# Kernel optimization log

Measured on AMD Instinct MI355X. Metric: run time of the kernel, lower is better.

The kernel has to match this reference:

```python
import jax, jax.numpy as jnp
import numpy as np
from functools import partial

REGION_NUM = 5
ALPHA = 0.02


def _otsu(u8, N):
    """Per-batch Otsu threshold. u8: (B, N) int32 in [0,255] -> (B,) int32.
    Matches cv2.THRESH_OTSU: argmax over t of between-class variance with
    class0 = bins <= t, binarization is pixel > t."""
    B = u8.shape[0]
    hist = jnp.zeros((B, 256), jnp.float32).at[jnp.arange(B)[:, None], u8].add(1.0)
    p = hist / N
    bins = jnp.arange(256, dtype=jnp.float32)
    w0 = jnp.cumsum(p, axis=1)                 # class-0 mass up to bin t
    mu = jnp.cumsum(p * bins, axis=1)          # class-0 first moment
    mu_t = mu[:, -1:]                          # total mean
    sigma_b = (mu_t * w0 - mu) ** 2 / (w0 * (1.0 - w0) + 1e-12)
    return jnp.argmax(sigma_b, axis=1)         # first max, like OpenCV


def _cc_label(mask):
    """8-connected components via iterative min-label propagation.
    mask: (H, W) bool -> (H, W) int32 labels; 0 = background, components get
    the (min flat index + 1) of their pixels as a unique id in 1..N."""
    H, W = mask.shape
    N = H * W
    BIG = jnp.int32(N + 1)
    idx = jnp.arange(1, N + 1, dtype=jnp.int32).reshape(H, W)
    lab0 = jnp.where(mask, idx, BIG)

    def step(l):
        p = jnp.pad(l, 1, constant_values=N + 1)
        nb = jnp.stack([p[i:i + H, j:j + W] for i in range(3) for j in range(3)])
        return jnp.where(mask, jnp.min(nb, axis=0), BIG)

    def cond(s):
        _, changed, it = s
        return changed & (it < N)

    def body(s):
        l, _, it = s
        nl = step(l)
        return (nl, jnp.any(nl != l), it + 1)

    lab, _, _ = jax.lax.while_loop(cond, body, (lab0, jnp.bool_(True), jnp.int32(0)))
    return jnp.where(mask, lab, 0)


def _forward(z, query_z):
    B, N, D = z.shape
    H = W = int(round(N ** 0.5))
    K = REGION_NUM - 1

    # similarity score + per-batch min-max normalization
    sim = jnp.einsum('bd,bnd->bn', query_z[:, 0], z) / (D ** 0.5)   # (B, N)
    smin = jnp.min(sim, axis=1, keepdims=True)
    smax = jnp.max(sim, axis=1, keepdims=True)
    sal = (sim - smin) / (smax - smin + 1e-6)
    sal = jax.lax.stop_gradient(sal)  # torch detaches before the numpy/cv2 pipeline

    # uint8 quantization (truncation, like .astype(np.uint8)) + Otsu binarization
    u8 = jnp.clip(jnp.floor(sal * 255.0), 0, 255).astype(jnp.int32)
    t = _otsu(u8, N)                              # (B,)
    binary = u8 > t[:, None]                      # (B, N) bool

    # connected components per image
    labels = jax.vmap(_cc_label)(binary.reshape(B, H, W)).reshape(B, N)  # 0..N

    # per-component area and mean saliency
    seg = partial(jax.ops.segment_sum, num_segments=N + 1)
    area = jax.vmap(seg)(jnp.ones((B, N), jnp.float32), labels)   # (B, N+1)
    ssum = jax.vmap(seg)(sal, labels)                              # (B, N+1)
    mean = ssum / jnp.maximum(area, 1.0)

    # keep components with area >= ALPHA*N (label 0 = non-mask excluded)
    valid = (area >= ALPHA * N) & (jnp.arange(N + 1) > 0)
    cand = jnp.where(valid, mean, -jnp.inf)

    # top-(region_num-1) components by mean saliency
    top_s, top_l = jax.lax.top_k(cand, K)         # (B, K)
    sel = jnp.isfinite(top_s)                     # (B, K)
    region = (labels[:, None, :] == top_l[:, :, None]) & sel[:, :, None]  # (B, K, N)
    bg = ~jnp.any(region, axis=1)                 # background = complement of union
    return jnp.concatenate([region, bg[:, None, :]], axis=1).astype(z.dtype)


def setup_inputs() -> dict:
    key = jax.random.key(0)
    k1, k2 = jax.random.split(key)
    B, N, D = 64, 1024, 768
    return {
        'z': jax.random.normal(k1, (B, N, D), dtype=jnp.float32),
        'query_z': jax.random.normal(k2, (B, 1, D), dtype=jnp.float32),
    }


def reference(z, query_z):
    return _forward(z, query_z)
```

## Files before the change

### kernel.cpp

```cpp
#include <hip/hip_runtime.h>
#include <stdint.h>

#define NB   64
#define NPIX 1024
#define DIM  768
#define KTOP 4

__global__ __launch_bounds__(256) void sgatt_sim(const float* __restrict__ z,
                                                 const float* __restrict__ q,
                                                 float* __restrict__ sim) {
    const int b    = blockIdx.y;
    const int lane = threadIdx.x & 63;
    const int wave = threadIdx.x >> 6;
    const float4* qv = reinterpret_cast<const float4*>(q + (size_t)b * DIM);
    const float4 q0 = qv[lane], q1 = qv[lane + 64], q2 = qv[lane + 128];
    const float rt = sqrtf((float)DIM);
#pragma unroll
    for (int r = 0; r < 4; ++r) {
        const int row = blockIdx.x * 16 + wave * 4 + r;
        const float4* zv =
            reinterpret_cast<const float4*>(z + (size_t)(b * NPIX + row) * DIM);
        const float4 z0 = zv[lane], z1 = zv[lane + 64], z2 = zv[lane + 128];
        double acc = (double)z0.x * q0.x + (double)z0.y * q0.y +
                     (double)z0.z * q0.z + (double)z0.w * q0.w;
        acc += (double)z1.x * q1.x + (double)z1.y * q1.y +
               (double)z1.z * q1.z + (double)z1.w * q1.w;
        acc += (double)z2.x * q2.x + (double)z2.y * q2.y +
               (double)z2.z * q2.z + (double)z2.w * q2.w;
#pragma unroll
        for (int o = 32; o > 0; o >>= 1) acc += __shfl_xor(acc, o);
        if (lane == 0) sim[b * NPIX + row] = (float)acc / rt;
    }
}

__device__ inline int uf_find(volatile int* p, int x) {
    int px = p[x];
    while (px != x) {
        const int g = p[px];
        if (g != px) p[x] = g;
        x = g;
        px = p[x];
    }
    return x;
}

__device__ inline void uf_union(volatile int* p, int a, int b) {
    while (true) {
        a = uf_find(p, a);
        b = uf_find(p, b);
        if (a == b) return;
        const int hi = a > b ? a : b;
        const int lo = a ^ b ^ hi;
        const int old = atomicCAS((int*)&p[hi], hi, lo);
        if (old == hi) return;
        a = old; b = lo;
    }
}

__global__ __launch_bounds__(256) void sgatt_region(const float* __restrict__ sim,
                                                    float* __restrict__ out) {
    const int b    = blockIdx.x;
    const int t    = threadIdx.x;
    const int lane = t & 63;
    const int wid  = t >> 6;

    __shared__ int   s_bufA[NPIX];
    __shared__ int   s_bufB[NPIX];
    __shared__ float s_wA[4], s_wB[4];
    __shared__ float s_avv[4];
    __shared__ int   s_avi[4];
    __shared__ float s_smin, s_smax;
    __shared__ int   s_thr;
    __shared__ int   s_top[KTOP];

    s_bufB[t] = 0;
    if (t < NPIX / 32) s_bufB[256 + t] = 0;
    int* s_hist = s_bufB;
    unsigned int* s_mbits = reinterpret_cast<unsigned int*>(s_bufB + 256);

    const float4 sv4 =
        reinterpret_cast<const float4*>(sim + (size_t)b * NPIX)[t];
    const float svj[4] = {sv4.x, sv4.y, sv4.z, sv4.w};
    float mn = fminf(fminf(svj[0], svj[1]), fminf(svj[2], svj[3]));
    float mx = fmaxf(fmaxf(svj[0], svj[1]), fmaxf(svj[2], svj[3]));
#pragma unroll
    for (int o = 32; o > 0; o >>= 1) {
        mn = fminf(mn, __shfl_xor(mn, o));
        mx = fmaxf(mx, __shfl_xor(mx, o));
    }
    if (lane == 0) { s_wA[wid] = mn; s_wB[wid] = mx; }
    __syncthreads();
    if (t == 0) {
        float a = s_wA[0], c = s_wB[0];
        for (int w = 1; w < 4; ++w) { a = fminf(a, s_wA[w]); c = fmaxf(c, s_wB[w]); }
        s_smin = a; s_smax = c;
    }
    __syncthreads();

    const float smin = s_smin;
    const float den0 = __fadd_rn(__fsub_rn(s_smax, smin), 1e-6f);
    float salj[4];
    int u8j[4];
#pragma unroll
    for (int j = 0; j < 4; ++j) {
        salj[j] = __fdiv_rn(__fsub_rn(svj[j], smin), den0);
        int u = (int)floorf(__fmul_rn(salj[j], 255.0f));
        u8j[j] = min(max(u, 0), 255);
        atomicAdd(&s_hist[u8j[j]], 1);
    }
    __syncthreads();

    {
        const float p = __fmul_rn((float)s_hist[t], 1.0f / 1024.0f);
        float w0 = p;
        float mu = __fmul_rn(p, (float)t);
#pragma unroll
        for (int o = 1; o < 64; o <<= 1) {
            const float aw = __shfl_up(w0, o);
            const float am = __shfl_up(mu, o);
            if (lane >= o) { w0 = __fadd_rn(w0, aw); mu = __fadd_rn(mu, am); }
        }
        if (lane == 63) { s_wA[wid] = w0; s_wB[wid] = mu; }
        __syncthreads();
        float mut = 0.0f;
        for (int w = 0; w < 4; ++w) mut = __fadd_rn(mut, s_wB[w]);
        for (int w = 0; w < wid; ++w) {
            w0 = __fadd_rn(w0, s_wA[w]);
            mu = __fadd_rn(mu, s_wB[w]);
        }
        const float num = __fsub_rn(__fmul_rn(mut, w0), mu);
        const float dn  = __fadd_rn(__fmul_rn(w0, __fsub_rn(1.0f, w0)), 1e-12f);
        float v  = __fdiv_rn(__fmul_rn(num, num), dn);
        int   idx = t;
#pragma unroll
        for (int o = 32; o > 0; o >>= 1) {
            const float v2 = __shfl_xor(v, o);
            const int   i2 = __shfl_xor(idx, o);
            if (v2 > v || (v2 == v && i2 < idx)) { v = v2; idx = i2; }
        }
        if (lane == 0) { s_avv[wid] = v; s_avi[wid] = idx; }
    }
    __syncthreads();
    if (t == 0) {
        float bv = s_avv[0]; int bi = s_avi[0];
        for (int w = 1; w < 4; ++w)
            if (s_avv[w] > bv || (s_avv[w] == bv && s_avi[w] < bi)) {
                bv = s_avv[w]; bi = s_avi[w];
            }
        s_thr = bi;
    }
    __syncthreads();
    const int thr = s_thr;

    int* s_par = s_bufA;
    int mj[4];
#pragma unroll
    for (int j = 0; j < 4; ++j) {
        const int px = 4*t + j;
        mj[j] = (u8j[j] > thr) ? 1 : 0;
        s_par[px] = (j > 0 && mj[j] && mj[j-1]) ? (px - 1) : px;
        if (mj[j]) atomicOr(&s_mbits[px >> 5], 1u << (px & 31));
    }
    __syncthreads();

#pragma unroll
    for (int j = 0; j < 4; ++j) {
        if (!mj[j]) continue;
        const int px = 4*t + j;
        const int r = px >> 5, c = px & 31;
#define ONMASK(p) ((s_mbits[(p) >> 5] >> ((p) & 31)) & 1u)
        if (j == 0 && c > 0 && ONMASK(px - 1)) uf_union(s_par, px, px - 1);
        if (r > 0) {
            if (c > 0 && ONMASK(px - 33)) uf_union(s_par, px, px - 33);
            if (ONMASK(px - 32))          uf_union(s_par, px, px - 32);
            if (c < 31 && ONMASK(px - 31)) uf_union(s_par, px, px - 31);
        }
#undef ONMASK
    }
    __syncthreads();

    int labj[4];
    {
        int cur[4], par[4];
#pragma unroll
        for (int j = 0; j < 4; ++j) cur[j] = 4*t + j;
#pragma unroll
        for (int j = 0; j < 4; ++j) par[j] = s_par[cur[j]];
        while (true) {
            bool any = false;
#pragma unroll
            for (int j = 0; j < 4; ++j) any |= (par[j] != cur[j]);
            if (!any) break;
#pragma unroll
            for (int j = 0; j < 4; ++j) cur[j] = par[j];
#pragma unroll
            for (int j = 0; j < 4; ++j) par[j] = s_par[cur[j]];
        }
#pragma unroll
        for (int j = 0; j < 4; ++j) labj[j] = mj[j] ? (cur[j] + 1) : 0;
    }
    __syncthreads();

    float* s_ssum = reinterpret_cast<float*>(s_bufA);
    int*   s_area = s_bufB;
#pragma unroll
    for (int j = 0; j < 4; ++j) { s_area[4*t + j] = 0; s_ssum[4*t + j] = 0.0f; }
    __syncthreads();
#pragma unroll
    for (int j = 0; j < 4; ++j) {
        if (mj[j]) {
            atomicAdd(&s_area[labj[j] - 1], 1);
            atomicAdd(&s_ssum[labj[j] - 1], salj[j]);
        }
    }
    __syncthreads();

    if (wid == 0) {
        unsigned long long key[16];
#pragma unroll
        for (int i = 0; i < 16; ++i) {
            const int idx = lane * 16 + i;
            const int a = s_area[idx];
            key[i] = 0ull;
            if (a >= 21) {
                const float mean = __fdiv_rn(s_ssum[idx], (float)a);
                key[i] = ((unsigned long long)__float_as_uint(mean) << 32) |
                         (unsigned long long)(0xFFFFFFFFu - (unsigned)(idx + 1));
            }
        }
        for (int k = 0; k < KTOP; ++k) {
            unsigned long long v = key[0];
#pragma unroll
            for (int i = 1; i < 16; ++i) v = (key[i] > v) ? key[i] : v;
#pragma unroll
            for (int o = 32; o > 0; o >>= 1) {
                const unsigned long long w = __shfl_xor(v, o);
                if (w > v) v = w;
            }
            if (lane == 0)
                s_top[k] = (v != 0ull)
                               ? (int)(0xFFFFFFFFu - (unsigned)(v & 0xFFFFFFFFull))
                               : -1;
#pragma unroll
            for (int i = 0; i < 16; ++i)
                if (key[i] == v && v != 0ull) key[i] = 0ull;
        }
    }
    __syncthreads();

    float* ob = out + (size_t)b * 5 * NPIX;
    int anyr[4] = {0, 0, 0, 0};
#pragma unroll
    for (int k = 0; k < KTOP; ++k) {
        const int tl = s_top[k];
        float4 o;
        float* op = reinterpret_cast<float*>(&o);
#pragma unroll
        for (int j = 0; j < 4; ++j) {
            const int match = (tl >= 0 && labj[j] == tl) ? 1 : 0;
            anyr[j] |= match;
            op[j] = (float)match;
        }
        reinterpret_cast<float4*>(ob + (size_t)k * NPIX)[t] = o;
    }
    {
        float4 o;
        float* op = reinterpret_cast<float*>(&o);
#pragma unroll
        for (int j = 0; j < 4; ++j) op[j] = anyr[j] ? 0.0f : 1.0f;
        reinterpret_cast<float4*>(ob + (size_t)KTOP * NPIX)[t] = o;
    }
}

extern "C" void kernel_launch(void* const* d_in, const int* in_sizes, int n_in,
                              void* d_out, int out_size, void* d_ws, size_t ws_size,
                              hipStream_t stream) {
    const float* z = (const float*)d_in[0];
    const float* q = (const float*)d_in[1];
    float* out = (float*)d_out;
    float* sim = (float*)d_ws;

    dim3 g1(NPIX / 16, NB);
    sgatt_sim<<<g1, 256, 0, stream>>>(z, q, sim);
    sgatt_region<<<NB, 256, 0, stream>>>(sim, out);
}
```

Before: 56.84 us.

## Run region kernel as a single wavefront per batch with shuffle-based top-k

Shrinks the per-batch region kernel from 256 threads (4 waves) to one 64-lane wavefront handling 16 pixels per lane. Cross-wave reductions for min/max, the Otsu scan and the argmax become pure wave shuffles, which drops several shared-memory round trips and block barriers. The serial 4-pass top-k is replaced by a per-lane sorted top-4 merged with a shuffle bitonic-style network. The trade-off is less parallelism per block: more serial work per lane and more registers, while only 64 blocks of 64 threads run on the GPU.

```diff
diff --git a/kernel.cpp b/kernel.cpp
--- a/kernel.cpp
+++ b/kernel.cpp
@@ -57,218 +57,256 @@
     }
 }
 
-__global__ __launch_bounds__(256) void sgatt_region(const float* __restrict__ sim,
-                                                    float* __restrict__ out) {
-    const int b    = blockIdx.x;
-    const int t    = threadIdx.x;
-    const int lane = t & 63;
-    const int wid  = t >> 6;
-
-    __shared__ int   s_bufA[NPIX];
-    __shared__ int   s_bufB[NPIX];
-    __shared__ float s_wA[4], s_wB[4];
-    __shared__ float s_avv[4];
-    __shared__ int   s_avi[4];
-    __shared__ float s_smin, s_smax;
-    __shared__ int   s_thr;
-    __shared__ int   s_top[KTOP];
-
-    s_bufB[t] = 0;
-    if (t < NPIX / 32) s_bufB[256 + t] = 0;
+__device__ inline unsigned long long umax64(unsigned long long a,
+                                            unsigned long long b) {
+    return a > b ? a : b;
+}
+__device__ inline unsigned long long umin64(unsigned long long a,
+                                            unsigned long long b) {
+    return a < b ? a : b;
+}
+
+__global__ __launch_bounds__(64) void sgatt_region(const float* __restrict__ sim,
+                                                   float* __restrict__ out) {
+    const int b = blockIdx.x;
+    const int l = threadIdx.x;
+
+    __shared__ int s_bufA[NPIX];
+    __shared__ int s_bufB[NPIX];
+
+    s_bufB[l] = 0; s_bufB[l + 64] = 0; s_bufB[l + 128] = 0; s_bufB[l + 192] = 0;
+    if (l < 32) s_bufB[256 + l] = 0;
     int* s_hist = s_bufB;
     unsigned int* s_mbits = reinterpret_cast<unsigned int*>(s_bufB + 256);
 
-    const float4 sv4 =
-        reinterpret_cast<const float4*>(sim + (size_t)b * NPIX)[t];
-    const float svj[4] = {sv4.x, sv4.y, sv4.z, sv4.w};
-    float mn = fminf(fminf(svj[0], svj[1]), fminf(svj[2], svj[3]));
-    float mx = fmaxf(fmaxf(svj[0], svj[1]), fmaxf(svj[2], svj[3]));
+    const float4* sb = reinterpret_cast<const float4*>(sim + (size_t)b * NPIX);
+    float svj[16];
+    {
+        const float4 v0 = sb[l], v1 = sb[l + 64], v2 = sb[l + 128],
+                     v3 = sb[l + 192];
+        svj[0]=v0.x; svj[1]=v0.y; svj[2]=v0.z; svj[3]=v0.w;
+        svj[4]=v1.x; svj[5]=v1.y; svj[6]=v1.z; svj[7]=v1.w;
+        svj[8]=v2.x; svj[9]=v2.y; svj[10]=v2.z; svj[11]=v2.w;
+        svj[12]=v3.x; svj[13]=v3.y; svj[14]=v3.z; svj[15]=v3.w;
+    }
+    float mn = svj[0], mx = svj[0];
+#pragma unroll
+    for (int i = 1; i < 16; ++i) {
+        mn = fminf(mn, svj[i]);
+        mx = fmaxf(mx, svj[i]);
+    }
 #pragma unroll
     for (int o = 32; o > 0; o >>= 1) {
         mn = fminf(mn, __shfl_xor(mn, o));
         mx = fmaxf(mx, __shfl_xor(mx, o));
     }
-    if (lane == 0) { s_wA[wid] = mn; s_wB[wid] = mx; }
-    __syncthreads();
-    if (t == 0) {
-        float a = s_wA[0], c = s_wB[0];
-        for (int w = 1; w < 4; ++w) { a = fminf(a, s_wA[w]); c = fmaxf(c, s_wB[w]); }
-        s_smin = a; s_smax = c;
-    }
-    __syncthreads();
-
-    const float smin = s_smin;
-    const float den0 = __fadd_rn(__fsub_rn(s_smax, smin), 1e-6f);
-    float salj[4];
-    int u8j[4];
-#pragma unroll
-    for (int j = 0; j < 4; ++j) {
-        salj[j] = __fdiv_rn(__fsub_rn(svj[j], smin), den0);
-        int u = (int)floorf(__fmul_rn(salj[j], 255.0f));
-        u8j[j] = min(max(u, 0), 255);
-        atomicAdd(&s_hist[u8j[j]], 1);
-    }
-    __syncthreads();
-
+
+    const float den0 = __fadd_rn(__fsub_rn(mx, mn), 1e-6f);
+    float salj[16];
+    int u8j[16];
+#pragma unroll
+    for (int i = 0; i < 16; ++i) {
+        salj[i] = __fdiv_rn(__fsub_rn(svj[i], mn), den0);
+        int u = (int)floorf(__fmul_rn(salj[i], 255.0f));
+        u8j[i] = min(max(u, 0), 255);
+    }
+    __syncthreads();
+#pragma unroll
+    for (int i = 0; i < 16; ++i) atomicAdd(&s_hist[u8j[i]], 1);
+    __syncthreads();
+
+    int thr;
     {
-        const float p = __fmul_rn((float)s_hist[t], 1.0f / 1024.0f);
-        float w0 = p;
-        float mu = __fmul_rn(p, (float)t);
+        const float p0 = __fmul_rn((float)s_hist[4*l + 0], 1.0f / 1024.0f);
+        const float p1 = __fmul_rn((float)s_hist[4*l + 1], 1.0f / 1024.0f);
+        const float p2 = __fmul_rn((float)s_hist[4*l + 2], 1.0f / 1024.0f);
+        const float p3 = __fmul_rn((float)s_hist[4*l + 3], 1.0f / 1024.0f);
+        const float cw0 = p0;
+        const float cw1 = __fadd_rn(cw0, p1);
+        const float cw2 = __fadd_rn(cw1, p2);
+        const float cw3 = __fadd_rn(cw2, p3);
+        const float q0 = __fmul_rn(p0, (float)(4*l + 0));
+        const float q1 = __fmul_rn(p1, (float)(4*l + 1));
+        const float q2 = __fmul_rn(p2, (float)(4*l + 2));
+        const float q3 = __fmul_rn(p3, (float)(4*l + 3));
+        const float cm0 = q0;
+        const float cm1 = __fadd_rn(cm0, q1);
+        const float cm2 = __fadd_rn(cm1, q2);
+        const float cm3 = __fadd_rn(cm2, q3);
+        float sw = cw3, sm = cm3;
 #pragma unroll
         for (int o = 1; o < 64; o <<= 1) {
-            const float aw = __shfl_up(w0, o);
-            const float am = __shfl_up(mu, o);
-            if (lane >= o) { w0 = __fadd_rn(w0, aw); mu = __fadd_rn(mu, am); }
-        }
-        if (lane == 63) { s_wA[wid] = w0; s_wB[wid] = mu; }
-        __syncthreads();
-        float mut = 0.0f;
-        for (int w = 0; w < 4; ++w) mut = __fadd_rn(mut, s_wB[w]);
-        for (int w = 0; w < wid; ++w) {
-            w0 = __fadd_rn(w0, s_wA[w]);
-            mu = __fadd_rn(mu, s_wB[w]);
-        }
-        const float num = __fsub_rn(__fmul_rn(mut, w0), mu);
-        const float dn  = __fadd_rn(__fmul_rn(w0, __fsub_rn(1.0f, w0)), 1e-12f);
-        float v  = __fdiv_rn(__fmul_rn(num, num), dn);
-        int   idx = t;
+            const float aw = __shfl_up(sw, o);
+            const float am = __shfl_up(sm, o);
+            if (l >= o) { sw = __fadd_rn(sw, aw); sm = __fadd_rn(sm, am); }
+        }
+        const float mut = __shfl(sm, 63);
+        const float pw = __fsub_rn(sw, cw3);
+        const float pm = __fsub_rn(sm, cm3);
+
+        float bv = -1.0f;
+        int bi = 4*l;
+        const float cw[4] = {cw0, cw1, cw2, cw3};
+        const float cm[4] = {cm0, cm1, cm2, cm3};
+#pragma unroll
+        for (int k = 0; k < 4; ++k) {
+            const float w0k = __fadd_rn(pw, cw[k]);
+            const float muk = __fadd_rn(pm, cm[k]);
+            const float num = __fsub_rn(__fmul_rn(mut, w0k), muk);
+            const float dnm =
+                __fadd_rn(__fmul_rn(w0k, __fsub_rn(1.0f, w0k)), 1e-12f);
+            const float v = __fdiv_rn(__fmul_rn(num, num), dnm);
+            if (v > bv) { bv = v; bi = 4*l + k; }
+        }
 #pragma unroll
         for (int o = 32; o > 0; o >>= 1) {
-            const float v2 = __shfl_xor(v, o);
-            const int   i2 = __shfl_xor(idx, o);
-            if (v2 > v || (v2 == v && i2 < idx)) { v = v2; idx = i2; }
-        }
-        if (lane == 0) { s_avv[wid] = v; s_avi[wid] = idx; }
-    }
-    __syncthreads();
-    if (t == 0) {
-        float bv = s_avv[0]; int bi = s_avi[0];
-        for (int w = 1; w < 4; ++w)
-            if (s_avv[w] > bv || (s_avv[w] == bv && s_avi[w] < bi)) {
-                bv = s_avv[w]; bi = s_avi[w];
-            }
-        s_thr = bi;
-    }
-    __syncthreads();
-    const int thr = s_thr;
+            const float v2 = __shfl_xor(bv, o);
+            const int   i2 = __shfl_xor(bi, o);
+            if (v2 > bv || (v2 == bv && i2 < bi)) { bv = v2; bi = i2; }
+        }
+        thr = bi;
+    }
 
     int* s_par = s_bufA;
-    int mj[4];
-#pragma unroll
-    for (int j = 0; j < 4; ++j) {
-        const int px = 4*t + j;
-        mj[j] = (u8j[j] > thr) ? 1 : 0;
-        s_par[px] = (j > 0 && mj[j] && mj[j-1]) ? (px - 1) : px;
-        if (mj[j]) atomicOr(&s_mbits[px >> 5], 1u << (px & 31));
-    }
-    __syncthreads();
-
-#pragma unroll
-    for (int j = 0; j < 4; ++j) {
-        if (!mj[j]) continue;
-        const int px = 4*t + j;
+    int mmask = 0;
+#pragma unroll
+    for (int i = 0; i < 16; ++i)
+        if (u8j[i] > thr) mmask |= (1 << i);
+#pragma unroll
+    for (int q = 0; q < 4; ++q) {
+        const int nib = (mmask >> (4*q)) & 0xF;
+#pragma unroll
+        for (int j = 0; j < 4; ++j) {
+            const int px = q*256 + 4*l + j;
+            const int on  = (nib >> j) & 1;
+            const int pon = (j > 0) ? ((nib >> (j - 1)) & 1) : 0;
+            s_par[px] = (on && pon) ? (px - 1) : px;
+        }
+        if (nib)
+            atomicOr(&s_mbits[(q*256 + 4*l) >> 5],
+                     (unsigned)nib << ((4*l) & 31));
+    }
+    __syncthreads();
+
+#define ONMASK(p) ((s_mbits[(p) >> 5] >> ((p) & 31)) & 1u)
+#pragma unroll
+    for (int i = 0; i < 16; ++i) {
+        if (!((mmask >> i) & 1)) continue;
+        const int px = ((i >> 2) << 8) + 4*l + (i & 3);
         const int r = px >> 5, c = px & 31;
-#define ONMASK(p) ((s_mbits[(p) >> 5] >> ((p) & 31)) & 1u)
-        if (j == 0 && c > 0 && ONMASK(px - 1)) uf_union(s_par, px, px - 1);
+        if ((i & 3) == 0 && c > 0 && ONMASK(px - 1)) uf_union(s_par, px, px - 1);
         if (r > 0) {
             if (c > 0 && ONMASK(px - 33)) uf_union(s_par, px, px - 33);
             if (ONMASK(px - 32))          uf_union(s_par, px, px - 32);
             if (c < 31 && ONMASK(px - 31)) uf_union(s_par, px, px - 31);
         }
+    }
 #undef ONMASK
-    }
-    __syncthreads();
-
-    int labj[4];
+    __syncthreads();
+
+    int labj[16];
     {
-        int cur[4], par[4];
-#pragma unroll
-        for (int j = 0; j < 4; ++j) cur[j] = 4*t + j;
-#pragma unroll
-        for (int j = 0; j < 4; ++j) par[j] = s_par[cur[j]];
+        int cur[16], par[16];
+#pragma unroll
+        for (int i = 0; i < 16; ++i) cur[i] = ((i >> 2) << 8) + 4*l + (i & 3);
+#pragma unroll
+        for (int i = 0; i < 16; ++i) par[i] = s_par[cur[i]];
         while (true) {
             bool any = false;
 #pragma unroll
-            for (int j = 0; j < 4; ++j) any |= (par[j] != cur[j]);
+            for (int i = 0; i < 16; ++i) any |= (par[i] != cur[i]);
             if (!any) break;
 #pragma unroll
-            for (int j = 0; j < 4; ++j) cur[j] = par[j];
-#pragma unroll
-            for (int j = 0; j < 4; ++j) par[j] = s_par[cur[j]];
-        }
-#pragma unroll
-        for (int j = 0; j < 4; ++j) labj[j] = mj[j] ? (cur[j] + 1) : 0;
+            for (int i = 0; i < 16; ++i) cur[i] = par[i];
+#pragma unroll
+            for (int i = 0; i < 16; ++i) par[i] = s_par[cur[i]];
+        }
+#pragma unroll
+        for (int i = 0; i < 16; ++i)
+            labj[i] = ((mmask >> i) & 1) ? (cur[i] + 1) : 0;
     }
     __syncthreads();
 
     float* s_ssum = reinterpret_cast<float*>(s_bufA);
     int*   s_area = s_bufB;
 #pragma unroll
-    for (int j = 0; j < 4; ++j) { s_area[4*t + j] = 0; s_ssum[4*t + j] = 0.0f; }
-    __syncthreads();
-#pragma unroll
-    for (int j = 0; j < 4; ++j) {
-        if (mj[j]) {
-            atomicAdd(&s_area[labj[j] - 1], 1);
-            atomicAdd(&s_ssum[labj[j] - 1], salj[j]);
-        }
-    }
-    __syncthreads();
-
-    if (wid == 0) {
-        unsigned long long key[16];
-#pragma unroll
-        for (int i = 0; i < 16; ++i) {
-            const int idx = lane * 16 + i;
-            const int a = s_area[idx];
-            key[i] = 0ull;
-            if (a >= 21) {
-                const float mean = __fdiv_rn(s_ssum[idx], (float)a);
-                key[i] = ((unsigned long long)__float_as_uint(mean) << 32) |
-                         (unsigned long long)(0xFFFFFFFFu - (unsigned)(idx + 1));
+    for (int i = 0; i < 16; ++i) { s_area[l + 64*i] = 0; s_ssum[l + 64*i] = 0.0f; }
+    __syncthreads();
+#pragma unroll
+    for (int i = 0; i < 16; ++i) {
+        if ((mmask >> i) & 1) {
+            atomicAdd(&s_area[labj[i] - 1], 1);
+            atomicAdd(&s_ssum[labj[i] - 1], salj[i]);
+        }
+    }
+    __syncthreads();
+
+    unsigned long long k0 = 0, k1 = 0, k2 = 0, k3 = 0;
+#pragma unroll
+    for (int i = 0; i < 16; ++i) {
+        const int idx = l + 64*i;
+        const int a = s_area[idx];
+        unsigned long long key = 0ull;
+        if (a >= 21) {
+            const float mean = __fdiv_rn(s_ssum[idx], (float)a);
+            key = ((unsigned long long)__float_as_uint(mean) << 32) |
+                  (unsigned long long)(0xFFFFFFFFu - (unsigned)(idx + 1));
+        }
+        const bool g0 = key > k0, g1 = key > k1, g2 = key > k2, g3 = key > k3;
+        const unsigned long long o0 = k0, o1 = k1, o2 = k2;
+        k0 = g0 ? key : k0;
+        k1 = g0 ? o0 : (g1 ? key : k1);
+        k2 = g1 ? o1 : (g2 ? key : k2);
+        k3 = g2 ? o2 : (g3 ? key : k3);
+    }
+#pragma unroll
+    for (int o = 32; o > 0; o >>= 1) {
+        const unsigned long long p0 = __shfl_xor(k0, o);
+        const unsigned long long p1 = __shfl_xor(k1, o);
+        const unsigned long long p2 = __shfl_xor(k2, o);
+        const unsigned long long p3 = __shfl_xor(k3, o);
+        const unsigned long long t0 = umax64(k0, p3);
+        const unsigned long long t1 = umax64(k1, p2);
+        const unsigned long long t2 = umax64(k2, p1);
+        const unsigned long long t3 = umax64(k3, p0);
+        const unsigned long long u0 = umax64(t0, t2), u2 = umin64(t0, t2);
+        const unsigned long long u1 = umax64(t1, t3), u3 = umin64(t1, t3);
+        k0 = umax64(u0, u1); k1 = umin64(u0, u1);
+        k2 = umax64(u2, u3); k3 = umin64(u2, u3);
+    }
+    int tlv[KTOP];
+    tlv[0] = k0 ? (int)(0xFFFFFFFFu - (unsigned)(k0 & 0xFFFFFFFFull)) : -1;
+    tlv[1] = k1 ? (int)(0xFFFFFFFFu - (unsigned)(k1 & 0xFFFFFFFFull)) : -1;
+    tlv[2] = k2 ? (int)(0xFFFFFFFFu - (unsigned)(k2 & 0xFFFFFFFFull)) : -1;
+    tlv[3] = k3 ? (int)(0xFFFFFFFFu - (unsigned)(k3 & 0xFFFFFFFFull)) : -1;
+
+    float* ob = out + (size_t)b * 5 * NPIX;
+    int anyr = 0;
+#pragma unroll
+    for (int k = 0; k < KTOP; ++k) {
+        const int tlk = tlv[k];
+#pragma unroll
+        for (int q = 0; q < 4; ++q) {
+            float4 o;
+            float* op = reinterpret_cast<float*>(&o);
+#pragma unroll
+            for (int j = 0; j < 4; ++j) {
+                const int i = 4*q + j;
+                const int match = (tlk >= 0 && labj[i] == tlk) ? 1 : 0;
+                anyr |= match << i;
+                op[j] = (float)match;
             }
-        }
-        for (int k = 0; k < KTOP; ++k) {
-            unsigned long long v = key[0];
-#pragma unroll
-            for (int i = 1; i < 16; ++i) v = (key[i] > v) ? key[i] : v;
-#pragma unroll
-            for (int o = 32; o > 0; o >>= 1) {
-                const unsigned long long w = __shfl_xor(v, o);
-                if (w > v) v = w;
-            }
-            if (lane == 0)
-                s_top[k] = (v != 0ull)
-                               ? (int)(0xFFFFFFFFu - (unsigned)(v & 0xFFFFFFFFull))
-                               : -1;
-#pragma unroll
-            for (int i = 0; i < 16; ++i)
-                if (key[i] == v && v != 0ull) key[i] = 0ull;
-        }
-    }
-    __syncthreads();
-
-    float* ob = out + (size_t)b * 5 * NPIX;
-    int anyr[4] = {0, 0, 0, 0};
-#pragma unroll
-    for (int k = 0; k < KTOP; ++k) {
-        const int tl = s_top[k];
+            reinterpret_cast<float4*>(ob + (size_t)k * NPIX + q*256)[l] = o;
+        }
+    }
+#pragma unroll
+    for (int q = 0; q < 4; ++q) {
         float4 o;
         float* op = reinterpret_cast<float*>(&o);
 #pragma unroll
-        for (int j = 0; j < 4; ++j) {
-            const int match = (tl >= 0 && labj[j] == tl) ? 1 : 0;
-            anyr[j] |= match;
-            op[j] = (float)match;
-        }
-        reinterpret_cast<float4*>(ob + (size_t)k * NPIX)[t] = o;
-    }
-    {
-        float4 o;
-        float* op = reinterpret_cast<float*>(&o);
-#pragma unroll
-        for (int j = 0; j < 4; ++j) op[j] = anyr[j] ? 0.0f : 1.0f;
-        reinterpret_cast<float4*>(ob + (size_t)KTOP * NPIX)[t] = o;
+        for (int j = 0; j < 4; ++j)
+            op[j] = ((anyr >> (4*q + j)) & 1) ? 0.0f : 1.0f;
+        reinterpret_cast<float4*>(ob + (size_t)KTOP * NPIX + q*256)[l] = o;
     }
 }
 
@@ -282,5 +320,5 @@
 
     dim3 g1(NPIX / 16, NB);
     sgatt_sim<<<g1, 256, 0, stream>>>(z, q, sim);
-    sgatt_region<<<NB, 256, 0, stream>>>(sim, out);
-}
+    sgatt_region<<<NB, 64, 0, stream>>>(sim, out);
+}
```

Measured after the change: 83.91 us. 1.48x slower.

## Cut barriers in region kernel with per-wave histograms and parallel top-k merge

Applied to the files above, without the earlier changes.

Restructures the region kernel to remove several block barriers. Histogram and segment-sum accumulation now go into per-wave privatized shared arrays, so the separate zeroing barriers disappear and atomic contention drops. Each thread reads the min/max and Otsu argmax reductions redundantly from shared memory instead of waiting for a single-thread step. The mask bitmap is replaced by packed u8 values, and top-4 selection is done by all waves with a sorting-network shuffle merge. The cost is much larger shared memory use, about 40KB per block, which may lower occupancy, plus extra zeroing stores.

```diff
diff --git a/kernel.cpp b/kernel.cpp
--- a/kernel.cpp
+++ b/kernel.cpp
@@ -57,6 +57,15 @@
     }
 }
 
+__device__ inline unsigned long long umax64(unsigned long long a,
+                                            unsigned long long b) {
+    return a > b ? a : b;
+}
+__device__ inline unsigned long long umin64(unsigned long long a,
+                                            unsigned long long b) {
+    return a < b ? a : b;
+}
+
 __global__ __launch_bounds__(256) void sgatt_region(const float* __restrict__ sim,
                                                     float* __restrict__ out) {
     const int b    = blockIdx.x;
@@ -64,41 +73,46 @@
     const int lane = t & 63;
     const int wid  = t >> 6;
 
-    __shared__ int   s_bufA[NPIX];
-    __shared__ int   s_bufB[NPIX];
+    __shared__ int   s_par[NPIX];
+    __shared__ int   s_hist[4 * 256];
+    __shared__ unsigned int s_u8p[256];
+    __shared__ int   s_areaw[4 * NPIX];
+    __shared__ float s_ssumw[4 * NPIX];
     __shared__ float s_wA[4], s_wB[4];
     __shared__ float s_avv[4];
     __shared__ int   s_avi[4];
-    __shared__ float s_smin, s_smax;
-    __shared__ int   s_thr;
-    __shared__ int   s_top[KTOP];
-
-    s_bufB[t] = 0;
-    if (t < NPIX / 32) s_bufB[256 + t] = 0;
-    int* s_hist = s_bufB;
-    unsigned int* s_mbits = reinterpret_cast<unsigned int*>(s_bufB + 256);
+    __shared__ unsigned long long s_part[16];
 
     const float4 sv4 =
         reinterpret_cast<const float4*>(sim + (size_t)b * NPIX)[t];
     const float svj[4] = {sv4.x, sv4.y, sv4.z, sv4.w};
-    float mn = fminf(fminf(svj[0], svj[1]), fminf(svj[2], svj[3]));
-    float mx = fmaxf(fmaxf(svj[0], svj[1]), fmaxf(svj[2], svj[3]));
-#pragma unroll
-    for (int o = 32; o > 0; o >>= 1) {
-        mn = fminf(mn, __shfl_xor(mn, o));
-        mx = fmaxf(mx, __shfl_xor(mx, o));
-    }
-    if (lane == 0) { s_wA[wid] = mn; s_wB[wid] = mx; }
-    __syncthreads();
-    if (t == 0) {
-        float a = s_wA[0], c = s_wB[0];
-        for (int w = 1; w < 4; ++w) { a = fminf(a, s_wA[w]); c = fmaxf(c, s_wB[w]); }
-        s_smin = a; s_smax = c;
-    }
-    __syncthreads();
-
-    const float smin = s_smin;
-    const float den0 = __fadd_rn(__fsub_rn(s_smax, smin), 1e-6f);
+    {
+        float mn = fminf(fminf(svj[0], svj[1]), fminf(svj[2], svj[3]));
+        float mx = fmaxf(fmaxf(svj[0], svj[1]), fmaxf(svj[2], svj[3]));
+#pragma unroll
+        for (int o = 32; o > 0; o >>= 1) {
+            mn = fminf(mn, __shfl_xor(mn, o));
+            mx = fmaxf(mx, __shfl_xor(mx, o));
+        }
+        if (lane == 0) { s_wA[wid] = mn; s_wB[wid] = mx; }
+    }
+#pragma unroll
+    for (int k = 0; k < 4; ++k) s_hist[t + 256 * k] = 0;
+#pragma unroll
+    for (int k = 0; k < 16; ++k) {
+        s_areaw[t + 256 * k] = 0;
+        s_ssumw[t + 256 * k] = 0.0f;
+    }
+    __syncthreads();
+
+    float smin = s_wA[0], smax = s_wB[0];
+#pragma unroll
+    for (int w = 1; w < 4; ++w) {
+        smin = fminf(smin, s_wA[w]);
+        smax = fmaxf(smax, s_wB[w]);
+    }
+
+    const float den0 = __fadd_rn(__fsub_rn(smax, smin), 1e-6f);
     float salj[4];
     int u8j[4];
 #pragma unroll
@@ -106,77 +120,87 @@
         salj[j] = __fdiv_rn(__fsub_rn(svj[j], smin), den0);
         int u = (int)floorf(__fmul_rn(salj[j], 255.0f));
         u8j[j] = min(max(u, 0), 255);
-        atomicAdd(&s_hist[u8j[j]], 1);
-    }
-    __syncthreads();
-
-    {
-        const float p = __fmul_rn((float)s_hist[t], 1.0f / 1024.0f);
-        float w0 = p;
-        float mu = __fmul_rn(p, (float)t);
+    }
+    s_u8p[t] = (unsigned)u8j[0] | ((unsigned)u8j[1] << 8) |
+               ((unsigned)u8j[2] << 16) | ((unsigned)u8j[3] << 24);
+    {
+        int* hw = s_hist + wid * 256;
+#pragma unroll
+        for (int j = 0; j < 4; ++j) atomicAdd(&hw[u8j[j]], 1);
+    }
+    __syncthreads();
+
+    int thr;
+    {
+        const int hsum = s_hist[t] + s_hist[t + 256] + s_hist[t + 512] +
+                         s_hist[t + 768];
+        const float p = __fmul_rn((float)hsum, 1.0f / 1024.0f);
+        float sw = p;
+        float sm = __fmul_rn(p, (float)t);
+        const float ownw = sw, ownm = sm;
+        (void)ownw; (void)ownm;
 #pragma unroll
         for (int o = 1; o < 64; o <<= 1) {
-            const float aw = __shfl_up(w0, o);
-            const float am = __shfl_up(mu, o);
-            if (lane >= o) { w0 = __fadd_rn(w0, aw); mu = __fadd_rn(mu, am); }
-        }
-        if (lane == 63) { s_wA[wid] = w0; s_wB[wid] = mu; }
+            const float aw = __shfl_up(sw, o);
+            const float am = __shfl_up(sm, o);
+            if (lane >= o) { sw = __fadd_rn(sw, aw); sm = __fadd_rn(sm, am); }
+        }
+        if (lane == 63) { s_wA[wid] = sw; s_wB[wid] = sm; }
         __syncthreads();
-        float mut = 0.0f;
-        for (int w = 0; w < 4; ++w) mut = __fadd_rn(mut, s_wB[w]);
+        float mut = s_wB[0];
+#pragma unroll
+        for (int w = 1; w < 4; ++w) mut = __fadd_rn(mut, s_wB[w]);
         for (int w = 0; w < wid; ++w) {
-            w0 = __fadd_rn(w0, s_wA[w]);
-            mu = __fadd_rn(mu, s_wB[w]);
-        }
-        const float num = __fsub_rn(__fmul_rn(mut, w0), mu);
-        const float dn  = __fadd_rn(__fmul_rn(w0, __fsub_rn(1.0f, w0)), 1e-12f);
-        float v  = __fdiv_rn(__fmul_rn(num, num), dn);
-        int   idx = t;
+            sw = __fadd_rn(sw, s_wA[w]);
+            sm = __fadd_rn(sm, s_wB[w]);
+        }
+        const float num = __fsub_rn(__fmul_rn(mut, sw), sm);
+        const float dnm =
+            __fadd_rn(__fmul_rn(sw, __fsub_rn(1.0f, sw)), 1e-12f);
+        float bv = __fdiv_rn(__fmul_rn(num, num), dnm);
+        int   bi = t;
 #pragma unroll
         for (int o = 32; o > 0; o >>= 1) {
-            const float v2 = __shfl_xor(v, o);
-            const int   i2 = __shfl_xor(idx, o);
-            if (v2 > v || (v2 == v && i2 < idx)) { v = v2; idx = i2; }
-        }
-        if (lane == 0) { s_avv[wid] = v; s_avi[wid] = idx; }
-    }
-    __syncthreads();
-    if (t == 0) {
-        float bv = s_avv[0]; int bi = s_avi[0];
-        for (int w = 1; w < 4; ++w)
-            if (s_avv[w] > bv || (s_avv[w] == bv && s_avi[w] < bi)) {
-                bv = s_avv[w]; bi = s_avi[w];
-            }
-        s_thr = bi;
-    }
-    __syncthreads();
-    const int thr = s_thr;
-
-    int* s_par = s_bufA;
+            const float v2 = __shfl_xor(bv, o);
+            const int   i2 = __shfl_xor(bi, o);
+            if (v2 > bv || (v2 == bv && i2 < bi)) { bv = v2; bi = i2; }
+        }
+        if (lane == 0) { s_avv[wid] = bv; s_avi[wid] = bi; }
+        __syncthreads();
+        float fv = s_avv[0];
+        int   fi = s_avi[0];
+#pragma unroll
+        for (int w = 1; w < 4; ++w) {
+            const float v2 = s_avv[w];
+            const int   i2 = s_avi[w];
+            if (v2 > fv || (v2 == fv && i2 < fi)) { fv = v2; fi = i2; }
+        }
+        thr = fi;
+    }
+
     int mj[4];
 #pragma unroll
     for (int j = 0; j < 4; ++j) {
         const int px = 4*t + j;
         mj[j] = (u8j[j] > thr) ? 1 : 0;
         s_par[px] = (j > 0 && mj[j] && mj[j-1]) ? (px - 1) : px;
-        if (mj[j]) atomicOr(&s_mbits[px >> 5], 1u << (px & 31));
-    }
-    __syncthreads();
-
+    }
+    __syncthreads();
+
+#define ONPX(p) ((int)((s_u8p[(p) >> 2] >> (((p) & 3) * 8)) & 255u) > thr)
 #pragma unroll
     for (int j = 0; j < 4; ++j) {
         if (!mj[j]) continue;
         const int px = 4*t + j;
         const int r = px >> 5, c = px & 31;
-#define ONMASK(p) ((s_mbits[(p) >> 5] >> ((p) & 31)) & 1u)
-        if (j == 0 && c > 0 && ONMASK(px - 1)) uf_union(s_par, px, px - 1);
+        if (j == 0 && c > 0 && ONPX(px - 1)) uf_union(s_par, px, px - 1);
         if (r > 0) {
-            if (c > 0 && ONMASK(px - 33)) uf_union(s_par, px, px - 33);
-            if (ONMASK(px - 32))          uf_union(s_par, px, px - 32);
-            if (c < 31 && ONMASK(px - 31)) uf_union(s_par, px, px - 31);
-        }
-#undef ONMASK
-    }
+            if (c > 0 && ONPX(px - 33)) uf_union(s_par, px, px - 33);
+            if (ONPX(px - 32))          uf_union(s_par, px, px - 32);
+            if (c < 31 && ONPX(px - 31)) uf_union(s_par, px, px - 31);
+        }
+    }
+#undef ONPX
     __syncthreads();
 
     int labj[4];
@@ -199,65 +223,101 @@
 #pragma unroll
         for (int j = 0; j < 4; ++j) labj[j] = mj[j] ? (cur[j] + 1) : 0;
     }
-    __syncthreads();
-
-    float* s_ssum = reinterpret_cast<float*>(s_bufA);
-    int*   s_area = s_bufB;
-#pragma unroll
-    for (int j = 0; j < 4; ++j) { s_area[4*t + j] = 0; s_ssum[4*t + j] = 0.0f; }
-    __syncthreads();
-#pragma unroll
-    for (int j = 0; j < 4; ++j) {
-        if (mj[j]) {
-            atomicAdd(&s_area[labj[j] - 1], 1);
-            atomicAdd(&s_ssum[labj[j] - 1], salj[j]);
-        }
-    }
-    __syncthreads();
-
-    if (wid == 0) {
-        unsigned long long key[16];
-#pragma unroll
-        for (int i = 0; i < 16; ++i) {
-            const int idx = lane * 16 + i;
-            const int a = s_area[idx];
-            key[i] = 0ull;
+    {
+        int*   aw = s_areaw + wid * NPIX;
+        float* sw = s_ssumw + wid * NPIX;
+#pragma unroll
+        for (int j = 0; j < 4; ++j) {
+            if (mj[j]) {
+                atomicAdd(&aw[labj[j] - 1], 1);
+                atomicAdd(&sw[labj[j] - 1], salj[j]);
+            }
+        }
+    }
+    __syncthreads();
+
+    unsigned long long k0 = 0, k1 = 0, k2 = 0, k3 = 0;
+    {
+        unsigned long long kk[4];
+#pragma unroll
+        for (int j = 0; j < 4; ++j) {
+            const int idx = 4*t + j;
+            const int a = s_areaw[idx] + s_areaw[idx + NPIX] +
+                          s_areaw[idx + 2*NPIX] + s_areaw[idx + 3*NPIX];
+            kk[j] = 0ull;
             if (a >= 21) {
-                const float mean = __fdiv_rn(s_ssum[idx], (float)a);
-                key[i] = ((unsigned long long)__float_as_uint(mean) << 32) |
-                         (unsigned long long)(0xFFFFFFFFu - (unsigned)(idx + 1));
+                const float ss =
+                    __fadd_rn(__fadd_rn(s_ssumw[idx], s_ssumw[idx + NPIX]),
+                              __fadd_rn(s_ssumw[idx + 2*NPIX],
+                                        s_ssumw[idx + 3*NPIX]));
+                const float mean = __fdiv_rn(ss, (float)a);
+                kk[j] = ((unsigned long long)__float_as_uint(mean) << 32) |
+                        (unsigned long long)(0xFFFFFFFFu - (unsigned)(idx + 1));
             }
         }
+        unsigned long long a0, a1;
+        a0 = umax64(kk[0], kk[1]); a1 = umin64(kk[0], kk[1]);
+        kk[0] = a0; kk[1] = a1;
+        a0 = umax64(kk[2], kk[3]); a1 = umin64(kk[2], kk[3]);
+        kk[2] = a0; kk[3] = a1;
+        a0 = umax64(kk[0], kk[2]); a1 = umin64(kk[0], kk[2]);
+        kk[0] = a0; kk[2] = a1;
+        a0 = umax64(kk[1], kk[3]); a1 = umin64(kk[1], kk[3]);
+        kk[1] = a0; kk[3] = a1;
+        a0 = umax64(kk[1], kk[2]); a1 = umin64(kk[1], kk[2]);
+        kk[1] = a0; kk[2] = a1;
+        k0 = kk[0]; k1 = kk[1]; k2 = kk[2]; k3 = kk[3];
+    }
+#pragma unroll
+    for (int o = 32; o > 0; o >>= 1) {
+        const unsigned long long p0 = __shfl_xor(k0, o);
+        const unsigned long long p1 = __shfl_xor(k1, o);
+        const unsigned long long p2 = __shfl_xor(k2, o);
+        const unsigned long long p3 = __shfl_xor(k3, o);
+        const unsigned long long t0 = umax64(k0, p3);
+        const unsigned long long t1 = umax64(k1, p2);
+        const unsigned long long t2 = umax64(k2, p1);
+        const unsigned long long t3 = umax64(k3, p0);
+        const unsigned long long u0 = umax64(t0, t2), u2 = umin64(t0, t2);
+        const unsigned long long u1 = umax64(t1, t3), u3 = umin64(t1, t3);
+        k0 = umax64(u0, u1); k1 = umin64(u0, u1);
+        k2 = umax64(u2, u3); k3 = umin64(u2, u3);
+    }
+    if (lane == 0) {
+        s_part[wid * 4 + 0] = k0;
+        s_part[wid * 4 + 1] = k1;
+        s_part[wid * 4 + 2] = k2;
+        s_part[wid * 4 + 3] = k3;
+    }
+    __syncthreads();
+    int tlv[KTOP];
+    {
+        unsigned long long kk[16];
+#pragma unroll
+        for (int i = 0; i < 16; ++i) kk[i] = s_part[i];
+#pragma unroll
         for (int k = 0; k < KTOP; ++k) {
-            unsigned long long v = key[0];
-#pragma unroll
-            for (int i = 1; i < 16; ++i) v = (key[i] > v) ? key[i] : v;
-#pragma unroll
-            for (int o = 32; o > 0; o >>= 1) {
-                const unsigned long long w = __shfl_xor(v, o);
-                if (w > v) v = w;
-            }
-            if (lane == 0)
-                s_top[k] = (v != 0ull)
-                               ? (int)(0xFFFFFFFFu - (unsigned)(v & 0xFFFFFFFFull))
-                               : -1;
+            unsigned long long v = kk[0];
+#pragma unroll
+            for (int i = 1; i < 16; ++i) v = umax64(v, kk[i]);
+            tlv[k] = v ? (int)(0xFFFFFFFFu - (unsigned)(v & 0xFFFFFFFFull))
+                       : -1;
 #pragma unroll
             for (int i = 0; i < 16; ++i)
-                if (key[i] == v && v != 0ull) key[i] = 0ull;
-        }
-    }
-    __syncthreads();
+                if (kk[i] == v && v != 0ull) kk[i] = 0ull;
+        }
+    }
 
     float* ob = out + (size_t)b * 5 * NPIX;
     int anyr[4] = {0, 0, 0, 0};
 #pragma unroll
     for (int k = 0; k < KTOP; ++k) {
-        const int tl = s_top[k];
+        const int tlk = tlv[k];
         float4 o;
         float* op = reinterpret_cast<float*>(&o);
 #pragma unroll
         for (int j = 0; j < 4; ++j) {
-            const int match = (tl >= 0 && labj[j] == tl) ? 1 : 0;
+            const int match = (tlk >= 0 && labj[j] == tlk) ? 1 : 0;
             anyr[j] |= match;
             op[j] = (float)match;
         }
```

After: 55.81 us. About the same (-1.8%).
